# Performance work log

Hardware: AMD Instinct MI355X
Metric: run time of the kernel (lower is better)

## Reference

```python
import jax, jax.numpy as jnp
import numpy as np

EPS = 1e-5

def _ada_ln(x, t, W, b):
    # NOTE: original code defines SiLU but never applies it in forward -> faithful: plain linear.
    emb = t @ W + b                       # (b, 1, 2*dim)
    scale, shift = jnp.split(emb, 2, axis=-1)
    mu = x.mean(-1, keepdims=True)
    var = ((x - mu) ** 2).mean(-1, keepdims=True)
    xn = (x - mu) * jax.lax.rsqrt(var + EPS)   # LayerNorm, elementwise_affine=False
    return xn * (1.0 + scale) + shift

def _attn(x, ctx, Wq, Wk, Wv, Wo, bo, heads):
    b, n, _ = x.shape
    j = ctx.shape[1]
    q = (x @ Wq).reshape(b, n, heads, -1)      # (b, i, h, dh)
    k = (ctx @ Wk).reshape(b, j, heads, -1)
    v = (ctx @ Wv).reshape(b, j, heads, -1)
    scale = q.shape[-1] ** -0.5
    sim = jnp.einsum('bihd,bjhd->bhij', q, k) * scale
    attn = jax.nn.softmax(sim, axis=-1)
    out = jnp.einsum('bhij,bjhd->bihd', attn, v).reshape(b, n, -1)
    return out @ Wo + bo

def _ff(x, W1, b1, W2, b2):
    p = x @ W1 + b1                            # (b, n, 8*dim)
    a, gate = jnp.split(p, 2, axis=-1)
    return (a * jax.nn.gelu(gate, approximate=False)) @ W2 + b2

def setup_inputs() -> dict:
    key = jax.random.key(0)
    ks = jax.random.split(key, 32)
    B, N, D = 4, 2048, 1024
    J, CD = 256, 768
    H, DH = 16, 64
    INNER = H * DH           # 1024
    FF = 4 * D               # 4096
    w = lambda k, shp: jax.random.normal(k, shp, jnp.float32) * 0.02
    inp = {
        'x': jax.random.normal(ks[0], (B, N, D), jnp.float32),
        't': jax.random.normal(ks[1], (B, 1, D), jnp.float32),
        'context': jax.random.normal(ks[2], (B, J, CD), jnp.float32),
        # AdaLayerNorms (weights stored (in, out))
        'n1_w': w(ks[3], (D, 2 * D)), 'n1_b': jnp.zeros((2 * D,), jnp.float32),
        'n2_w': w(ks[4], (D, 2 * D)), 'n2_b': jnp.zeros((2 * D,), jnp.float32),
        'n3_w': w(ks[5], (D, 2 * D)), 'n3_b': jnp.zeros((2 * D,), jnp.float32),
        # attn1 (self)
        'q1': w(ks[6], (D, INNER)), 'k1': w(ks[7], (D, INNER)), 'v1': w(ks[8], (D, INNER)),
        'o1_w': w(ks[9], (INNER, D)), 'o1_b': jnp.zeros((D,), jnp.float32),
        # attn2 (cross)
        'q2': w(ks[10], (D, INNER)), 'k2': w(ks[11], (CD, INNER)), 'v2': w(ks[12], (CD, INNER)),
        'o2_w': w(ks[13], (INNER, D)), 'o2_b': jnp.zeros((D,), jnp.float32),
        # GEGLU FeedForward
        'ff_w1': w(ks[14], (D, 2 * FF)), 'ff_b1': jnp.zeros((2 * FF,), jnp.float32),
        'ff_w2': w(ks[15], (FF, D)), 'ff_b2': jnp.zeros((D,), jnp.float32),
    }
    return inp

def reference(x, t, context,
              n1_w, n1_b, n2_w, n2_b, n3_w, n3_b,
              q1, k1, v1, o1_w, o1_b,
              q2, k2, v2, o2_w, o2_b,
              ff_w1, ff_b1, ff_w2, ff_b2):
    H = 16
    h = _ada_ln(x, t, n1_w, n1_b)
    x = _attn(h, h, q1, k1, v1, o1_w, o1_b, H) + x
    h = _ada_ln(x, t, n2_w, n2_b)
    x = _attn(h, context, q2, k2, v2, o2_w, o2_b, H) + x
    h = _ada_ln(x, t, n3_w, n3_b)
    x = _ff(h, ff_w1, ff_b1, ff_w2, ff_b2) + x
    return x
```

## Files before the change

### kernel.cpp

```cpp
#include <hip/hip_runtime.h>
#include <hip/hip_bf16.h>
#include <stdint.h>

typedef unsigned short u16;
typedef __attribute__((ext_vector_type(8))) short bf16x8;
typedef __attribute__((ext_vector_type(4))) float f32x4;

__device__ __forceinline__ u16 f2bf(float f) {
  __hip_bfloat16 h = __float2bfloat16(f);
  return *reinterpret_cast<u16*>(&h);
}
__device__ __forceinline__ float bf2f(u16 v) {
  return __uint_as_float(((uint32_t)v) << 16);
}
__device__ __forceinline__ float exp2_fast(float x) {
  return __builtin_amdgcn_exp2f(x);
}

typedef __attribute__((address_space(1))) const uint32_t gu32;
typedef __attribute__((address_space(3))) uint32_t lu32;
__device__ __forceinline__ void gload16(const u16* g, u16* l) {
  __builtin_amdgcn_global_load_lds((gu32*)g, (lu32*)l, 16, 0, 0);
}

__global__ __launch_bounds__(256)
void wtrans_k(const float* __restrict__ W, u16* __restrict__ Wt, int K, int N) {
  __shared__ float tile[32][33];
  int n0 = blockIdx.x * 32, k0 = blockIdx.y * 32;
  int t = threadIdx.x;
  int c = t & 31, r4 = t >> 5;
#pragma unroll
  for (int s = 0; s < 4; ++s) {
    int kr = r4 + 8 * s;
    tile[kr][c] = W[(size_t)(k0 + kr) * N + n0 + c];
  }
  __syncthreads();
#pragma unroll
  for (int s = 0; s < 4; ++s) {
    int nr = r4 + 8 * s;
    Wt[(size_t)(n0 + nr) * K + k0 + c] = f2bf(tile[c][nr]);
  }
}

__global__ __launch_bounds__(256)
void cvt_bf16_k(const float* __restrict__ in, u16* __restrict__ out, int n4) {
  int i = blockIdx.x * 256 + threadIdx.x;
  if (i < n4) {
    float4 v = ((const float4*)in)[i];
    ushort4 o;
    o.x = f2bf(v.x); o.y = f2bf(v.y); o.z = f2bf(v.z); o.w = f2bf(v.w);
    ((ushort4*)out)[i] = o;
  }
}

__global__ __launch_bounds__(256)
void vtrans_k(const u16* __restrict__ V, int sv, u16* __restrict__ Vt, int Nkv) {
  __shared__ u16 Tl[64][72];
  const int bh = blockIdx.y, b = bh >> 4, hh = bh & 15;
  const int jt = blockIdx.x, t = threadIdx.x;
  const int ntile = Nkv >> 6;
  {
    int jr = t >> 2, part = t & 3;
    const u16* src = V + (size_t)(b * Nkv + jt * 64 + jr) * sv + hh * 64 + part * 16;
    *(uint4*)(&Tl[jr][part * 16]) = *(const uint4*)src;
    *(uint4*)(&Tl[jr][part * 16 + 8]) = *(const uint4*)(src + 8);
  }
  __syncthreads();
  int d = t >> 2, ch = t & 3;
  u16 ov[16];
#pragma unroll
  for (int e = 0; e < 16; ++e) {
    int jj = ch * 16 + e;
    ov[e] = Tl[jj ^ ((d & 7) << 3)][d];
  }
  u16* dst = Vt + ((size_t)bh * ntile + jt) * 4096 + d * 64 + ch * 16;
  *(uint4*)dst = *(uint4*)&ov[0];
  *(uint4*)(dst + 8) = *(uint4*)&ov[8];
}

__global__ __launch_bounds__(256)
void emb_all_k(const float* __restrict__ tin,
               const float* __restrict__ w0, const float* __restrict__ b0,
               const float* __restrict__ w1, const float* __restrict__ b1,
               const float* __restrict__ w2, const float* __restrict__ b2,
               float* __restrict__ emb) {
  int p = blockIdx.x >> 5, c = blockIdx.x & 31;
  int norm = p >> 2, b = p & 3;
  int t = threadIdx.x;
  int n = c * 64 + (t & 63), kc = t >> 6;
  const float* W = norm == 0 ? w0 : (norm == 1 ? w1 : w2);
  const float* Bv = norm == 0 ? b0 : (norm == 1 ? b1 : b2);
  const float* tr = tin + b * 1024 + kc * 256;
  const float* Wp = W + (size_t)(kc * 256) * 2048 + n;
  float acc = 0.f;
#pragma unroll 8
  for (int k = 0; k < 256; ++k) acc = fmaf(tr[k], Wp[(size_t)k * 2048], acc);
  __shared__ float red[256];
  red[t] = acc;
  __syncthreads();
  if (kc == 0)
    emb[p * 2048 + n] = red[t] + red[64 + t] + red[128 + t] + red[192 + t] + Bv[n];
}

__global__ __launch_bounds__(256)
void ada_ln_k(const float* __restrict__ x, const float* __restrict__ emb,
              u16* __restrict__ h) {
  int row = blockIdx.x;
  int b = row >> 11;
  int t = threadIdx.x;
  const float4* xr = (const float4*)(x + (size_t)row * 1024);
  float4 v = xr[t];
  float s = v.x + v.y + v.z + v.w;
  float s2 = v.x * v.x + v.y * v.y + v.z * v.z + v.w * v.w;
#pragma unroll
  for (int m = 1; m < 64; m <<= 1) { s += __shfl_xor(s, m); s2 += __shfl_xor(s2, m); }
  __shared__ float rs[4], rs2[4];
  int w = t >> 6;
  if ((t & 63) == 0) { rs[w] = s; rs2[w] = s2; }
  __syncthreads();
  s = rs[0] + rs[1] + rs[2] + rs[3];
  s2 = rs2[0] + rs2[1] + rs2[2] + rs2[3];
  float mu = s * (1.f / 1024.f);
  float var = s2 * (1.f / 1024.f) - mu * mu;
  float rstd = rsqrtf(var + 1e-5f);
  const float4* sc = (const float4*)(emb + b * 2048);
  const float4* sh = (const float4*)(emb + b * 2048 + 1024);
  float4 c = sc[t], f = sh[t];
  ushort4 o;
  o.x = f2bf((v.x - mu) * rstd * (1.f + c.x) + f.x);
  o.y = f2bf((v.y - mu) * rstd * (1.f + c.y) + f.y);
  o.z = f2bf((v.z - mu) * rstd * (1.f + c.z) + f.z);
  o.w = f2bf((v.w - mu) * rstd * (1.f + c.w) + f.w);
  ((ushort4*)(h + (size_t)row * 1024))[t] = o;
}

enum { EPI_BF16 = 0, EPI_BIAS_RES = 1, EPI_GEGLU = 2, EPI_QKV = 3 };
#define QSCALE 0.1803368801111244f

template <int EPI>
__device__ __forceinline__ void epi_store(float v, int col, size_t idx,
                                          u16* outb, float* outf,
                                          const float* res) {
  if (EPI == EPI_BF16) {
    outb[idx] = f2bf(v);
  } else if (EPI == EPI_QKV) {
    outb[idx] = f2bf(col < 1024 ? v * QSCALE : v);
  } else if (EPI == EPI_BIAS_RES) {
    outf[idx] = v + res[idx];
  } else {
    float a = bf2f(outb[idx]);
    float g = 0.5f * v * (1.0f + erff(v * 0.70710678118f));
    outb[idx] = f2bf(a * g);
  }
}

template <int EPI>
__global__ __launch_bounds__(256)
void gemm_k(const u16* __restrict__ A, int lda,
            const u16* __restrict__ Bt, int ldb,
            const float* __restrict__ bias,
            const float* __restrict__ res,
            u16* __restrict__ outb, float* __restrict__ outf,
            int N, int K) {
  __shared__ u16 As[2][128 * 32];
  __shared__ u16 Bs[2][128 * 32];
  int nbx = gridDim.x;
  int id = blockIdx.y * nbx + blockIdx.x;
  int nwg = nbx * gridDim.y;
  int swz = (nwg & 7) ? id : ((id & 7) * (nwg >> 3) + (id >> 3));
  const int m0 = (swz / nbx) * 128, n0 = (swz % nbx) * 128;
  const int t = threadIdx.x;
  const int l = t & 63, w = t >> 6, lg = l >> 4, li = l & 15;
  const int wm = w >> 1, wn = w & 1;
  const int c0 = w, c1 = w + 4;
  const int r0 = c0 * 16 + (l >> 2), r1 = c1 * 16 + (l >> 2);
  const int cc = (l & 3) * 8;
  const u16* ga0 = A + (size_t)(m0 + r0) * lda + cc;
  const u16* ga1 = A + (size_t)(m0 + r1) * lda + cc;
  const u16* gb0 = Bt + (size_t)(n0 + r0) * ldb + cc;
  const u16* gb1 = Bt + (size_t)(n0 + r1) * ldb + cc;
  f32x4 acc[4][4] = {};
  auto stage = [&](int p, int k0) {
    gload16(ga0 + k0, As[p] + c0 * 512);
    gload16(ga1 + k0, As[p] + c1 * 512);
    gload16(gb0 + k0, Bs[p] + c0 * 512);
    gload16(gb1 + k0, Bs[p] + c1 * 512);
  };
  stage(0, 0);
  __syncthreads();
  int p = 0;
  for (int k0 = 0; k0 < K; k0 += 32) {
    if (k0 + 32 < K) stage(p ^ 1, k0 + 32);
    bf16x8 af[4], bfr[4];
#pragma unroll
    for (int i = 0; i < 4; ++i) {
      af[i]  = *(const bf16x8*)(As[p] + (wm * 64 + i * 16 + li) * 32 + lg * 8);
      bfr[i] = *(const bf16x8*)(Bs[p] + (wn * 64 + i * 16 + li) * 32 + lg * 8);
    }
#pragma unroll
    for (int i = 0; i < 4; ++i)
#pragma unroll
      for (int j = 0; j < 4; ++j)
        acc[i][j] = __builtin_amdgcn_mfma_f32_16x16x32_bf16(af[i], bfr[j], acc[i][j], 0, 0, 0);
    __syncthreads();
    p ^= 1;
  }
#pragma unroll
  for (int j = 0; j < 4; ++j) {
    int col = n0 + wn * 64 + j * 16 + li;
    float bv = bias ? bias[col] : 0.f;
#pragma unroll
    for (int i = 0; i < 4; ++i) {
#pragma unroll
      for (int r = 0; r < 4; ++r) {
        int row = m0 + wm * 64 + i * 16 + lg * 4 + r;
        size_t idx = (size_t)row * N + col;
        epi_store<EPI>(acc[i][j][r] + bv, col, idx, outb, outf, res);
      }
    }
  }
}

__global__ __launch_bounds__(512)
void flash_k(const u16* __restrict__ Q, int sq, const u16* __restrict__ Kb, int skv,
             const u16* __restrict__ Vt, u16* __restrict__ O,
             int Nq, int Nkv) {
  __shared__ u16 Kl[2][4096];
  __shared__ u16 Vl[2][4096];
  __shared__ u16 Pl[8][16][72];
  const int t = threadIdx.x, w = t >> 6, l = t & 63, lg = l >> 4, li = l & 15;
  const int bh = blockIdx.y, b = bh >> 4, hh = bh & 15;
  const int i0 = blockIdx.x * 256;
  const int ntile = Nkv >> 6;
  const u16* qrow0 = Q + ((size_t)b * Nq + i0 + w * 32 + li) * sq + hh * 64;
  const u16* qrow1 = qrow0 + (size_t)16 * sq;
  bf16x8 qf[2][2];
  qf[0][0] = *(const bf16x8*)(qrow0 + lg * 8);
  qf[0][1] = *(const bf16x8*)(qrow0 + 32 + lg * 8);
  qf[1][0] = *(const bf16x8*)(qrow1 + lg * 8);
  qf[1][1] = *(const bf16x8*)(qrow1 + 32 + lg * 8);
  const int krow_in = l >> 3;
  const int kcol = ((l & 7) ^ (l >> 3)) * 8;
  const u16* kbase = Kb + (size_t)b * Nkv * skv + hh * 64 + kcol;
  const u16* vtb = Vt + ((size_t)bh * ntile) * 4096 + l * 8;
  f32x4 sden[2] = {};
  f32x4 of[2][4] = {};
  bf16x8 ones;
#pragma unroll
  for (int e = 0; e < 8; ++e) ones[e] = (short)0x3F80;
  int kx[2], vx[2];
#pragma unroll
  for (int hf = 0; hf < 2; ++hf)
    kx[hf] = ((hf * 64 + lg * 16) ^ ((li & 7) << 4)) >> 1;
#pragma unroll
  for (int ks = 0; ks < 2; ++ks)
    vx[ks] = (ks * 32 + lg * 8) ^ ((li & 7) << 3);
  const int px = (lg * 8) ^ (((li >> 3) & 1) << 3);
  auto stage = [&](int p, int jt) {
    gload16(kbase + (size_t)(jt * 64 + w * 8 + krow_in) * skv, Kl[p] + w * 512);
    gload16(vtb + (size_t)jt * 4096 + w * 512, Vl[p] + w * 512);
  };
  stage(0, 0);
  __syncthreads();
  int p = 0;
  for (int jt = 0; jt < ntile; ++jt) {
    if (jt + 1 < ntile) stage(p ^ 1, jt + 1);
    const u16* Kp = Kl[p] + li * 64;
    const u16* Vp = Vl[p] + li * 64;
#pragma unroll
    for (int q = 0; q < 2; ++q) {
      f32x4 sacc[4] = {};
      __builtin_amdgcn_s_setprio(1);
#pragma unroll
      for (int nt = 0; nt < 4; ++nt) {
        bf16x8 k0 = *(const bf16x8*)(Kp + nt * 1024 + kx[0]);
        bf16x8 k1 = *(const bf16x8*)(Kp + nt * 1024 + kx[1]);
        sacc[nt] = __builtin_amdgcn_mfma_f32_16x16x32_bf16(qf[q][0], k0, sacc[nt], 0, 0, 0);
        sacc[nt] = __builtin_amdgcn_mfma_f32_16x16x32_bf16(qf[q][1], k1, sacc[nt], 0, 0, 0);
      }
      __builtin_amdgcn_s_setprio(0);
#pragma unroll
      for (int nt = 0; nt < 4; ++nt)
#pragma unroll
        for (int r = 0; r < 4; ++r) {
          float pe = exp2_fast(fminf(sacc[nt][r], 60.f));
          int prow = lg * 4 + r;
          Pl[w][prow][(nt * 16 + li) ^ (((prow >> 3) & 1) << 3)] = f2bf(pe);
        }
      __builtin_amdgcn_s_setprio(1);
#pragma unroll
      for (int ks = 0; ks < 2; ++ks) {
        bf16x8 pa = *(const bf16x8*)(&Pl[w][li][ks * 32 + px]);
#pragma unroll
        for (int nt = 0; nt < 4; ++nt) {
          bf16x8 vf = *(const bf16x8*)(Vp + nt * 1024 + vx[ks]);
          of[q][nt] = __builtin_amdgcn_mfma_f32_16x16x32_bf16(pa, vf, of[q][nt], 0, 0, 0);
        }
        sden[q] = __builtin_amdgcn_mfma_f32_16x16x32_bf16(pa, ones, sden[q], 0, 0, 0);
      }
      __builtin_amdgcn_s_setprio(0);
    }
    __syncthreads();
    p ^= 1;
  }
#pragma unroll
  for (int q = 0; q < 2; ++q)
#pragma unroll
    for (int r = 0; r < 4; ++r) {
      float inv = 1.f / sden[q][r];
      int row = i0 + w * 32 + q * 16 + lg * 4 + r;
      u16* orow = O + ((size_t)b * Nq + row) * 1024 + hh * 64;
#pragma unroll
      for (int nt = 0; nt < 4; ++nt)
        orow[nt * 16 + li] = f2bf(of[q][nt][r] * inv);
    }
}

extern "C" void kernel_launch(void* const* d_in, const int* in_sizes, int n_in,
                              void* d_out, int out_size, void* d_ws, size_t ws_size,
                              hipStream_t stream) {
  const float* X   = (const float*)d_in[0];
  const float* T   = (const float*)d_in[1];
  const float* CTX = (const float*)d_in[2];
  const float* N1W = (const float*)d_in[3];
  const float* N1B = (const float*)d_in[4];
  const float* N2W = (const float*)d_in[5];
  const float* N2B = (const float*)d_in[6];
  const float* N3W = (const float*)d_in[7];
  const float* N3B = (const float*)d_in[8];
  const float* Q1  = (const float*)d_in[9];
  const float* K1  = (const float*)d_in[10];
  const float* V1  = (const float*)d_in[11];
  const float* O1W = (const float*)d_in[12];
  const float* O1B = (const float*)d_in[13];
  const float* Q2  = (const float*)d_in[14];
  const float* K2  = (const float*)d_in[15];
  const float* V2  = (const float*)d_in[16];
  const float* O2W = (const float*)d_in[17];
  const float* O2B = (const float*)d_in[18];
  const float* FW1 = (const float*)d_in[19];
  const float* FB1 = (const float*)d_in[20];
  const float* FW2 = (const float*)d_in[21];
  const float* FB2 = (const float*)d_in[22];
  float* OUT = (float*)d_out;

  char* ws = (char*)d_ws;
  const size_t MB = 1ull << 20;
  u16* wt_q1 = (u16*)(ws + 0 * MB);
  u16* wt_k1 = (u16*)(ws + 2 * MB);
  u16* wt_v1 = (u16*)(ws + 4 * MB);
  u16* wt_o1 = (u16*)(ws + 6 * MB);
  u16* wt_q2 = (u16*)(ws + 8 * MB);
  u16* wt_k2 = (u16*)(ws + 10 * MB);
  u16* wt_v2 = (u16*)(ws + 10 * MB + 1536 * 1024);
  u16* wt_o2 = (u16*)(ws + 13 * MB);
  u16* wt_f1 = (u16*)(ws + 16 * MB);
  u16* wt_f2 = (u16*)(ws + 32 * MB);
  u16* ctxb  = (u16*)(ws + 40 * MB);
  float* emb = (float*)(ws + 42 * MB);
  u16* hbuf  = (u16*)(ws + 43 * MB);
  u16* vtbuf = (u16*)(ws + 43 * MB);
  u16* QKVb  = (u16*)(ws + 59 * MB);
  u16* Qb    = (u16*)(ws + 59 * MB);
  u16* KVb   = (u16*)(ws + 75 * MB);
  u16* AOb   = (u16*)(ws + 107 * MB);
  u16* abuf  = (u16*)(ws + 59 * MB);

  wtrans_k<<<dim3(32, 32), 256, 0, stream>>>(Q1, wt_q1, 1024, 1024);
  wtrans_k<<<dim3(32, 32), 256, 0, stream>>>(K1, wt_k1, 1024, 1024);
  wtrans_k<<<dim3(32, 32), 256, 0, stream>>>(V1, wt_v1, 1024, 1024);
  wtrans_k<<<dim3(32, 32), 256, 0, stream>>>(O1W, wt_o1, 1024, 1024);
  wtrans_k<<<dim3(32, 32), 256, 0, stream>>>(Q2, wt_q2, 1024, 1024);
  wtrans_k<<<dim3(32, 24), 256, 0, stream>>>(K2, wt_k2, 768, 1024);
  wtrans_k<<<dim3(32, 24), 256, 0, stream>>>(V2, wt_v2, 768, 1024);
  wtrans_k<<<dim3(32, 32), 256, 0, stream>>>(O2W, wt_o2, 1024, 1024);
  wtrans_k<<<dim3(256, 32), 256, 0, stream>>>(FW1, wt_f1, 1024, 8192);
  wtrans_k<<<dim3(32, 128), 256, 0, stream>>>(FW2, wt_f2, 4096, 1024);
  cvt_bf16_k<<<768, 256, 0, stream>>>(CTX, ctxb, 196608);
  emb_all_k<<<384, 256, 0, stream>>>(T, N1W, N1B, N2W, N2B, N3W, N3B, emb);

  ada_ln_k<<<8192, 256, 0, stream>>>(X, emb + 0, hbuf);
  gemm_k<EPI_QKV><<<dim3(24, 64), 256, 0, stream>>>(hbuf, 1024, wt_q1, 1024, nullptr, nullptr, QKVb, nullptr, 3072, 1024);
  vtrans_k<<<dim3(32, 64), 256, 0, stream>>>(QKVb + 2048, 3072, vtbuf, 2048);
  flash_k<<<dim3(8, 64), 512, 0, stream>>>(QKVb, 3072, QKVb + 1024, 3072, vtbuf, AOb, 2048, 2048);
  gemm_k<EPI_BIAS_RES><<<dim3(8, 64), 256, 0, stream>>>(AOb, 1024, wt_o1, 1024, O1B, X, nullptr, OUT, 1024, 1024);

  ada_ln_k<<<8192, 256, 0, stream>>>(OUT, emb + 8192, hbuf);
  gemm_k<EPI_QKV><<<dim3(8, 64), 256, 0, stream>>>(hbuf, 1024, wt_q2, 1024, nullptr, nullptr, Qb, nullptr, 1024, 1024);
  gemm_k<EPI_BF16><<<dim3(16, 8), 256, 0, stream>>>(ctxb, 768, wt_k2, 768, nullptr, nullptr, KVb, nullptr, 2048, 768);
  vtrans_k<<<dim3(4, 64), 256, 0, stream>>>(KVb + 1024, 2048, vtbuf, 256);
  flash_k<<<dim3(8, 64), 512, 0, stream>>>(Qb, 1024, KVb, 2048, vtbuf, AOb, 2048, 256);
  gemm_k<EPI_BIAS_RES><<<dim3(8, 64), 256, 0, stream>>>(AOb, 1024, wt_o2, 1024, O2B, OUT, nullptr, OUT, 1024, 1024);

  ada_ln_k<<<8192, 256, 0, stream>>>(OUT, emb + 16384, hbuf);
  gemm_k<EPI_BF16><<<dim3(32, 64), 256, 0, stream>>>(hbuf, 1024, wt_f1, 1024, FB1, nullptr, abuf, nullptr, 4096, 1024);
  gemm_k<EPI_GEGLU><<<dim3(32, 64), 256, 0, stream>>>(hbuf, 1024, wt_f1 + (size_t)4096 * 1024, 1024, FB1 + 4096, nullptr, abuf, nullptr, 4096, 1024);
  gemm_k<EPI_BIAS_RES><<<dim3(8, 64), 256, 0, stream>>>(abuf, 4096, wt_f2, 4096, FB2, OUT, nullptr, OUT, 1024, 4096);
}
```

Before: 681.1 us.

## Fuse GEGLU value and gate GEMMs into one dual-B kernel; widen QKV tiles

Adds a gemm2_k kernel that loads one A tile and two B tiles per k-step, accumulating two output tiles with 512 threads. The GEGLU feedforward now computes value and gate halves in one pass and applies bias and GELU in registers, removing the second GEMM launch, the re-read of hbuf, and the bf16 round trip of the value half through abuf. The QKV projection uses the same kernel with 128x256 tiles, halving the grid. Each thread now holds more accumulator registers, which may lower occupancy.

After: 633.0 us. 1.08x faster.

```diff
diff --git a/kernel.cpp b/kernel.cpp
--- a/kernel.cpp
+++ b/kernel.cpp
@@ -147,10 +147,6 @@
     outb[idx] = f2bf(col < 1024 ? v * QSCALE : v);
   } else if (EPI == EPI_BIAS_RES) {
     outf[idx] = v + res[idx];
-  } else {
-    float a = bf2f(outb[idx]);
-    float g = 0.5f * v * (1.0f + erff(v * 0.70710678118f));
-    outb[idx] = f2bf(a * g);
   }
 }
 
@@ -221,6 +217,92 @@
   }
 }
 
+template <int EPI>
+__global__ __launch_bounds__(512)
+void gemm2_k(const u16* __restrict__ A, int lda,
+             const u16* __restrict__ Bt, int ldb, int roff2,
+             const float* __restrict__ bias,
+             u16* __restrict__ outb, int N, int K) {
+  __shared__ u16 As[2][4096];
+  __shared__ u16 B0s[2][4096];
+  __shared__ u16 B1s[2][4096];
+  int nbx = gridDim.x;
+  int id = blockIdx.y * nbx + blockIdx.x;
+  int nwg = nbx * gridDim.y;
+  int swz = (nwg & 7) ? id : ((id & 7) * (nwg >> 3) + (id >> 3));
+  const int m0 = (swz / nbx) * 128;
+  const int n0 = (swz % nbx) * (EPI == EPI_QKV ? 256 : 128);
+  const int t = threadIdx.x;
+  const int w = t >> 6, l = t & 63, lg = l >> 4, li = l & 15;
+  const int wm = w >> 2, wn = w & 3;
+  const int sr = (w << 4) + (l >> 2), sc = (l & 3) * 8;
+  const u16* ga  = A  + (size_t)(m0 + sr) * lda + sc;
+  const u16* gb0 = Bt + (size_t)(n0 + sr) * ldb + sc;
+  const u16* gb1 = Bt + (size_t)(n0 + roff2 + sr) * ldb + sc;
+  const int ldst = w * 512;
+  f32x4 acc0[4][2] = {}, acc1[4][2] = {};
+  auto stage = [&](int p, int k0) {
+    gload16(ga + k0, As[p] + ldst);
+    gload16(gb0 + k0, B0s[p] + ldst);
+    gload16(gb1 + k0, B1s[p] + ldst);
+  };
+  stage(0, 0);
+  __syncthreads();
+  int p = 0;
+  for (int k0 = 0; k0 < K; k0 += 32) {
+    if (k0 + 32 < K) stage(p ^ 1, k0 + 32);
+    bf16x8 af[4], b0[2], b1[2];
+#pragma unroll
+    for (int i = 0; i < 4; ++i)
+      af[i] = *(const bf16x8*)(As[p] + (wm * 64 + i * 16 + li) * 32 + lg * 8);
+#pragma unroll
+    for (int j = 0; j < 2; ++j) {
+      b0[j] = *(const bf16x8*)(B0s[p] + (wn * 32 + j * 16 + li) * 32 + lg * 8);
+      b1[j] = *(const bf16x8*)(B1s[p] + (wn * 32 + j * 16 + li) * 32 + lg * 8);
+    }
+#pragma unroll
+    for (int i = 0; i < 4; ++i)
+#pragma unroll
+      for (int j = 0; j < 2; ++j) {
+        acc0[i][j] = __builtin_amdgcn_mfma_f32_16x16x32_bf16(af[i], b0[j], acc0[i][j], 0, 0, 0);
+        acc1[i][j] = __builtin_amdgcn_mfma_f32_16x16x32_bf16(af[i], b1[j], acc1[i][j], 0, 0, 0);
+      }
+    __syncthreads();
+    p ^= 1;
+  }
+#pragma unroll
+  for (int j = 0; j < 2; ++j) {
+    int cw = wn * 32 + j * 16 + li;
+    if (EPI == EPI_QKV) {
+#pragma unroll
+      for (int sub = 0; sub < 2; ++sub) {
+        int col = n0 + sub * 128 + cw;
+#pragma unroll
+        for (int i = 0; i < 4; ++i)
+#pragma unroll
+          for (int r = 0; r < 4; ++r) {
+            int row = m0 + wm * 64 + i * 16 + lg * 4 + r;
+            float v = sub ? acc1[i][j][r] : acc0[i][j][r];
+            outb[(size_t)row * N + col] = f2bf(col < 1024 ? v * QSCALE : v);
+          }
+      }
+    } else {
+      int col = n0 + cw;
+      float ba = bias[col], bg = bias[col + roff2];
+#pragma unroll
+      for (int i = 0; i < 4; ++i)
+#pragma unroll
+        for (int r = 0; r < 4; ++r) {
+          int row = m0 + wm * 64 + i * 16 + lg * 4 + r;
+          float a = acc0[i][j][r] + ba;
+          float g = acc1[i][j][r] + bg;
+          float gl = 0.5f * g * (1.0f + erff(g * 0.70710678118f));
+          outb[(size_t)row * N + col] = f2bf(a * gl);
+        }
+    }
+  }
+}
+
 __global__ __launch_bounds__(512)
 void flash_k(const u16* __restrict__ Q, int sq, const u16* __restrict__ Kb, int skv,
              const u16* __restrict__ Vt, u16* __restrict__ O,
@@ -380,7 +462,7 @@
   emb_all_k<<<384, 256, 0, stream>>>(T, N1W, N1B, N2W, N2B, N3W, N3B, emb);
 
   ada_ln_k<<<8192, 256, 0, stream>>>(X, emb + 0, hbuf);
-  gemm_k<EPI_QKV><<<dim3(24, 64), 256, 0, stream>>>(hbuf, 1024, wt_q1, 1024, nullptr, nullptr, QKVb, nullptr, 3072, 1024);
+  gemm2_k<EPI_QKV><<<dim3(12, 64), 512, 0, stream>>>(hbuf, 1024, wt_q1, 1024, 128, nullptr, QKVb, 3072, 1024);
   vtrans_k<<<dim3(32, 64), 256, 0, stream>>>(QKVb + 2048, 3072, vtbuf, 2048);
   flash_k<<<dim3(8, 64), 512, 0, stream>>>(QKVb, 3072, QKVb + 1024, 3072, vtbuf, AOb, 2048, 2048);
   gemm_k<EPI_BIAS_RES><<<dim3(8, 64), 256, 0, stream>>>(AOb, 1024, wt_o1, 1024, O1B, X, nullptr, OUT, 1024, 1024);
@@ -393,7 +475,6 @@
   gemm_k<EPI_BIAS_RES><<<dim3(8, 64), 256, 0, stream>>>(AOb, 1024, wt_o2, 1024, O2B, OUT, nullptr, OUT, 1024, 1024);
 
   ada_ln_k<<<8192, 256, 0, stream>>>(OUT, emb + 16384, hbuf);
-  gemm_k<EPI_BF16><<<dim3(32, 64), 256, 0, stream>>>(hbuf, 1024, wt_f1, 1024, FB1, nullptr, abuf, nullptr, 4096, 1024);
-  gemm_k<EPI_GEGLU><<<dim3(32, 64), 256, 0, stream>>>(hbuf, 1024, wt_f1 + (size_t)4096 * 1024, 1024, FB1 + 4096, nullptr, abuf, nullptr, 4096, 1024);
+  gemm2_k<EPI_GEGLU><<<dim3(32, 64), 512, 0, stream>>>(hbuf, 1024, wt_f1, 1024, 4096, FB1, abuf, 4096, 1024);
   gemm_k<EPI_BIAS_RES><<<dim3(8, 64), 256, 0, stream>>>(abuf, 4096, wt_f2, 4096, FB2, OUT, nullptr, OUT, 1024, 4096);
 }
```
